# Kernel optimization log

Measured on AMD Instinct MI355X. Metric: run time of the kernel, lower is better.

Reference implementation:

```python
import jax, jax.numpy as jnp
import numpy as np

D = 512      # d_model
P = 128      # proj_len
H = 8        # nhead
MID = 24     # middle_dim (hardcoded in module)
HD = MID // H    # head_dim = 3
HDV = D // H     # head_dim_v = 64
SCALE = HD ** -0.5   # scaling == pscaling since head_dim == phead_dim


def setup_inputs() -> dict:
    key = jax.random.key(0)
    ks = jax.random.split(key, 12)
    L, B = 2048, 16
    def w(k, o, i):
        return jax.random.normal(k, (o, i), jnp.float32) * 0.02
    def b(o):
        return jnp.zeros((o,), jnp.float32)
    return {
        "x": jax.random.normal(ks[0], (L, B, D), jnp.float32),
        "px": jax.random.normal(ks[1], (P, B, D), jnp.float32),
        "mask": jax.random.randint(ks[2], (B, L), 0, 2).astype(bool),
        "Wpq": w(ks[3], MID, D), "bpq": b(MID),
        "Wq": w(ks[4], MID, D), "bq": b(MID),
        "Wql": w(ks[5], P * H, D), "bql": b(P * H),
        "Wpk": w(ks[6], MID, D), "bpk": b(MID),
        "Wpv": w(ks[7], D, D), "bpv": b(D),
        "Wk": w(ks[8], MID, D), "bk": b(MID),
        "Wv": w(ks[9], D, D), "bv": b(D),
        "Wo": w(ks[10], D, D), "bo": b(D),
        "gamma": jnp.ones((D,), jnp.float32),
        "beta": jnp.zeros((D,), jnp.float32),
    }


def _layernorm(x, g, b, eps=1e-5):
    m = x.mean(-1, keepdims=True)
    v = ((x - m) ** 2).mean(-1, keepdims=True)
    return (x - m) / jnp.sqrt(v + eps) * g + b


def reference(x, px, mask, Wpq, bpq, Wq, bq, Wql, bql, Wpk, bpk, Wpv, bpv,
              Wk, bk, Wv, bv, Wo, bo, gamma, beta):
    L, B, _ = x.shape
    BH = B * H
    # ---- stage 1: compress length L -> P via projected attention ----
    pk = (x @ Wpk.T + bpk).reshape(L, BH, HD)     # [L, BH, hd]
    pv = (x @ Wpv.T + bpv).reshape(L, BH, HDV)    # [L, BH, hdv]
    pq = (px @ Wpq.T + bpq).reshape(P, BH, HD) * SCALE
    pqk = jnp.einsum('pnh,lnh->npl', pq, pk)      # [BH, P, L]
    pqk = pqk.reshape(B, H, P, L)
    pqk = jnp.where(mask[:, None, None, :], -jnp.inf, pqk).reshape(BH, P, L)
    pqk = jax.nn.softmax(pqk, axis=-1)            # dropout1 omitted (eval)
    pc = jnp.einsum('npl,lnv->npv', pqk, pv)      # [BH, P, hdv]
    pc = pc.transpose(1, 0, 2).reshape(P, B, D)   # compressed context
    # ---- stage 2: attention within compressed length P ----
    q_len = (x @ Wql.T + bql).reshape(L, BH, P).transpose(1, 0, 2)  # [BH, L, P]
    k = (pc @ Wk.T + bk).reshape(P, BH, HD).transpose(1, 0, 2)      # [BH, P, hd]
    v = (pc @ Wv.T + bv).reshape(P, BH, HDV).transpose(1, 0, 2)     # [BH, P, hdv]
    q = ((pc @ Wq.T + bq) * SCALE).reshape(P, BH, HD).transpose(1, 0, 2)
    aw = jax.nn.softmax(q @ k.transpose(0, 2, 1), axis=-1)  # [BH, P, P], dropout2 omitted
    attn = aw @ v                                            # [BH, P, hdv]
    attn = attn.transpose(1, 0, 2).reshape(P, B, D)
    attn = _layernorm(attn, gamma, beta)
    attn = attn.reshape(P, BH, HDV).transpose(1, 0, 2)       # [BH, P, hdv]
    # ---- stage 3: re-expand P -> L via learned length softmax ----
    ql = jax.nn.softmax(q_len, axis=-1)                      # dropout3 omitted
    out = (ql @ attn).transpose(1, 0, 2).reshape(L, B, D)
    return (out @ Wo.T + bo, pc)
```

## Files before the change

### kernel.cpp

```cpp
#include <hip/hip_runtime.h>
#include <cstdint>

#define L_    2048
#define B_    16
#define D_    512
#define P_    128
#define H_    8
#define MID_  24
#define HD_   3
#define HDV_  64
#define BH_   128
#define SCALE_ 0.57735026918962576f
#define S1C   4
#define S1L   (L_ / S1C)

typedef short  short8  __attribute__((ext_vector_type(8)));
typedef short  short4v __attribute__((ext_vector_type(4)));
typedef float  f32x4   __attribute__((ext_vector_type(4)));

__device__ __forceinline__ short f2bf(float f) {
    unsigned u = __builtin_bit_cast(unsigned, f);
    unsigned r = (u + 0x7fffu + ((u >> 16) & 1u)) >> 16;
    return (short)(unsigned short)r;
}

__device__ __forceinline__ int swz8(int row, int chunk) {
    return row * 64 + ((chunk ^ (row & 7)) << 3);
}

__device__ __forceinline__ int swzP(int row, int g) {
    return row * 128 + ((g ^ (row & 7)) << 3);
}

__device__ __forceinline__ float block_reduce_sum_256(float v, volatile float* scratch) {
#pragma unroll
    for (int o = 32; o > 0; o >>= 1) v += __shfl_down(v, o, 64);
    int wid = threadIdx.x >> 6;
    if ((threadIdx.x & 63) == 0) scratch[wid] = v;
    __syncthreads();
    if (threadIdx.x == 0) scratch[4] = scratch[0] + scratch[1] + scratch[2] + scratch[3];
    __syncthreads();
    return scratch[4];
}

__global__ __launch_bounds__(256) void cvt_bf16(
    const float* __restrict__ src, short* __restrict__ dst, int n4)
{
    int i = blockIdx.x * 256 + threadIdx.x;
    if (i < n4) {
        float4 v = reinterpret_cast<const float4*>(src)[i];
        short4v o;
        o[0] = f2bf(v.x); o[1] = f2bf(v.y); o[2] = f2bf(v.z); o[3] = f2bf(v.w);
        reinterpret_cast<short4v*>(dst)[i] = o;
    }
}

__global__ __launch_bounds__(256) void proj24(
    const float* __restrict__ A, const float* __restrict__ W,
    const float* __restrict__ bias, float* __restrict__ C, float scale)
{
    const int lane = threadIdx.x & 63;
    const int cg   = __builtin_amdgcn_readfirstlane(threadIdx.x >> 6);
    const int row  = blockIdx.x * 64 + lane;
    const int c0   = cg * 6;
    const float* __restrict__ wb = W + (size_t)c0 * D_;
    const float* __restrict__ xr = A + (size_t)row * D_;

    float acc[6] = {0.f, 0.f, 0.f, 0.f, 0.f, 0.f};
    for (int kk = 0; kk < D_; kk += 8) {
        float4 x0 = *reinterpret_cast<const float4*>(xr + kk);
        float4 x1 = *reinterpret_cast<const float4*>(xr + kk + 4);
#pragma unroll
        for (int j = 0; j < 6; ++j) {
            float4 w0 = *reinterpret_cast<const float4*>(wb + j * D_ + kk);
            float4 w1 = *reinterpret_cast<const float4*>(wb + j * D_ + kk + 4);
            acc[j] = fmaf(x0.x, w0.x, fmaf(x0.y, w0.y, fmaf(x0.z, w0.z, fmaf(x0.w, w0.w, acc[j]))));
            acc[j] = fmaf(x1.x, w1.x, fmaf(x1.y, w1.y, fmaf(x1.z, w1.z, fmaf(x1.w, w1.w, acc[j]))));
        }
    }
#pragma unroll
    for (int j = 0; j < 6; ++j)
        C[(size_t)row * MID_ + c0 + j] = (acc[j] + bias[c0 + j]) * scale;
}

__global__ __launch_bounds__(256) void gemm_bias2(
    const float* __restrict__ A,
    const float* __restrict__ W0, const float* __restrict__ b0, float* __restrict__ C0, float s0,
    const float* __restrict__ W1, const float* __restrict__ b1, float* __restrict__ C1, float s1,
    int M, int N, int K)
{
    const float* W    = blockIdx.z ? W1 : W0;
    const float* bias = blockIdx.z ? b1 : b0;
    float*       C    = blockIdx.z ? C1 : C0;
    const float scale = blockIdx.z ? s1 : s0;

    __shared__ float As[32][36];
    __shared__ float Ws[64][36];
    const int t    = threadIdx.x;
    const int row0 = blockIdx.y * 32;
    const int col0 = blockIdx.x * 64;
    const int ty = t >> 4;
    const int tx = t & 15;
    const int lr  = t >> 3;
    const int lc4 = (t & 7) * 4;

    float acc[2][4] = {{0.f,0.f,0.f,0.f},{0.f,0.f,0.f,0.f}};

    for (int kk0 = 0; kk0 < K; kk0 += 32) {
        {
            float4 a = *reinterpret_cast<const float4*>(&A[(size_t)(row0 + lr) * K + kk0 + lc4]);
            *reinterpret_cast<float4*>(&As[lr][lc4]) = a;
        }
#pragma unroll
        for (int i = 0; i < 2; ++i) {
            int wr   = i * 32 + lr;
            int wcol = col0 + wr;
            float4 w = make_float4(0.f, 0.f, 0.f, 0.f);
            if (wcol < N)
                w = *reinterpret_cast<const float4*>(&W[(size_t)wcol * K + kk0 + lc4]);
            *reinterpret_cast<float4*>(&Ws[wr][lc4]) = w;
        }
        __syncthreads();
#pragma unroll
        for (int k4 = 0; k4 < 8; ++k4) {
            float4 a0 = *reinterpret_cast<const float4*>(&As[ty * 2][k4 * 4]);
            float4 a1 = *reinterpret_cast<const float4*>(&As[ty * 2 + 1][k4 * 4]);
#pragma unroll
            for (int ci = 0; ci < 4; ++ci) {
                float4 w = *reinterpret_cast<const float4*>(&Ws[ci * 16 + tx][k4 * 4]);
                acc[0][ci] += a0.x * w.x + a0.y * w.y + a0.z * w.z + a0.w * w.w;
                acc[1][ci] += a1.x * w.x + a1.y * w.y + a1.z * w.z + a1.w * w.w;
            }
        }
        __syncthreads();
    }
#pragma unroll
    for (int ri = 0; ri < 2; ++ri) {
        int r = row0 + ty * 2 + ri;
#pragma unroll
        for (int ci = 0; ci < 4; ++ci) {
            int c = col0 + ci * 16 + tx;
            if (c < N) C[(size_t)r * N + c] = (acc[ri][ci] + bias[c]) * scale;
        }
    }
}

__global__ __launch_bounds__(256) void gemm_mfma_bt(
    const float* __restrict__ A, const short* __restrict__ Wb,
    const float* __restrict__ bias, float* __restrict__ C,
    int M, int N, int K)
{
    __shared__ __align__(16) short As[128][40];
    __shared__ __align__(16) short Bs[64][40];
    const int t    = threadIdx.x;
    const int w    = t >> 6;
    const int lane = t & 63;
    const int q    = lane >> 4;
    const int l16  = lane & 15;
    const int row0 = blockIdx.y * 128;
    const int col0 = blockIdx.x * 64;

    const int ar = t >> 1;
    const int ac = (t & 1) * 16;
    const int br = t >> 2;
    const int bc = (t & 3) * 8;

    const f32x4 z = {0.f, 0.f, 0.f, 0.f};
    f32x4 acc[2][4];
#pragma unroll
    for (int i = 0; i < 2; ++i)
#pragma unroll
        for (int j = 0; j < 4; ++j) acc[i][j] = z;

    for (int kk = 0; kk < K; kk += 32) {
        {
            const float4* ap = reinterpret_cast<const float4*>(&A[(size_t)(row0 + ar) * K + kk + ac]);
            float4 v0 = ap[0], v1 = ap[1], v2 = ap[2], v3 = ap[3];
            short8 s0, s1;
            s0[0]=f2bf(v0.x); s0[1]=f2bf(v0.y); s0[2]=f2bf(v0.z); s0[3]=f2bf(v0.w);
            s0[4]=f2bf(v1.x); s0[5]=f2bf(v1.y); s0[6]=f2bf(v1.z); s0[7]=f2bf(v1.w);
            s1[0]=f2bf(v2.x); s1[1]=f2bf(v2.y); s1[2]=f2bf(v2.z); s1[3]=f2bf(v2.w);
            s1[4]=f2bf(v3.x); s1[5]=f2bf(v3.y); s1[6]=f2bf(v3.z); s1[7]=f2bf(v3.w);
            *reinterpret_cast<short8*>(&As[ar][ac])     = s0;
            *reinterpret_cast<short8*>(&As[ar][ac + 8]) = s1;
        }
        *reinterpret_cast<short8*>(&Bs[br][bc]) =
            *reinterpret_cast<const short8*>(&Wb[(size_t)(col0 + br) * K + kk + bc]);
        __syncthreads();

        short8 af[2], bf[4];
#pragma unroll
        for (int i = 0; i < 2; ++i)
            af[i] = *reinterpret_cast<const short8*>(&As[32 * w + i * 16 + l16][q * 8]);
#pragma unroll
        for (int ct = 0; ct < 4; ++ct)
            bf[ct] = *reinterpret_cast<const short8*>(&Bs[ct * 16 + l16][q * 8]);
#pragma unroll
        for (int i = 0; i < 2; ++i)
#pragma unroll
            for (int ct = 0; ct < 4; ++ct)
                acc[i][ct] = __builtin_amdgcn_mfma_f32_16x16x32_bf16(af[i], bf[ct], acc[i][ct], 0, 0, 0);
        __syncthreads();
    }

#pragma unroll
    for (int i = 0; i < 2; ++i) {
#pragma unroll
        for (int ct = 0; ct < 4; ++ct) {
            int col = col0 + ct * 16 + l16;
            float bv = bias[col];
#pragma unroll
            for (int r = 0; r < 4; ++r) {
                int row = row0 + 32 * w + i * 16 + q * 4 + r;
                C[(size_t)row * N + col] = acc[i][ct][r] + bv;
            }
        }
    }
}

template<bool BF16OUT>
__global__ __launch_bounds__(256) void gemm_bb(
    const short* __restrict__ Ab, const short* __restrict__ Wb,
    const float* __restrict__ bias, void* __restrict__ Cout,
    int M, int N, int K)
{
    __shared__ __align__(16) short As[128 * 64];
    __shared__ __align__(16) short Bs[128 * 64];
    const int t    = threadIdx.x;
    const int w    = t >> 6;
    const int lane = t & 63;
    const int q    = lane >> 4;
    const int l16  = lane & 15;

    const int gid  = blockIdx.x;
    const int nct  = N >> 7;
    const int xcd  = gid & 7;
    const int j    = gid >> 3;
    const int row0 = (xcd + 8 * (j / nct)) * 128;
    const int col0 = (j % nct) * 128;

    const int sr  = t >> 1;
    const int sc0 = (t & 1) * 4;

    const f32x4 z = {0.f, 0.f, 0.f, 0.f};
    f32x4 acc[2][8];
#pragma unroll
    for (int i = 0; i < 2; ++i)
#pragma unroll
        for (int jj = 0; jj < 8; ++jj) acc[i][jj] = z;

    for (int kk = 0; kk < K; kk += 64) {
        {
            const short* ap = &Ab[(size_t)(row0 + sr) * K + kk + sc0 * 8];
            const short* bp = &Wb[(size_t)(col0 + sr) * K + kk + sc0 * 8];
#pragma unroll
            for (int c = 0; c < 4; ++c) {
                *reinterpret_cast<short8*>(&As[swz8(sr, sc0 + c)]) =
                    *reinterpret_cast<const short8*>(ap + c * 8);
                *reinterpret_cast<short8*>(&Bs[swz8(sr, sc0 + c)]) =
                    *reinterpret_cast<const short8*>(bp + c * 8);
            }
        }
        __syncthreads();

        __builtin_amdgcn_s_setprio(1);
#pragma unroll
        for (int s = 0; s < 2; ++s) {
            short8 af[2], bf[8];
#pragma unroll
            for (int i = 0; i < 2; ++i)
                af[i] = *reinterpret_cast<const short8*>(&As[swz8(32 * w + i * 16 + l16, s * 4 + q)]);
#pragma unroll
            for (int ct = 0; ct < 8; ++ct)
                bf[ct] = *reinterpret_cast<const short8*>(&Bs[swz8(ct * 16 + l16, s * 4 + q)]);
#pragma unroll
            for (int i = 0; i < 2; ++i)
#pragma unroll
                for (int ct = 0; ct < 8; ++ct)
                    acc[i][ct] = __builtin_amdgcn_mfma_f32_16x16x32_bf16(af[i], bf[ct], acc[i][ct], 0, 0, 0);
        }
        __builtin_amdgcn_s_setprio(0);
        __syncthreads();
    }

#pragma unroll
    for (int i = 0; i < 2; ++i) {
#pragma unroll
        for (int ct = 0; ct < 8; ++ct) {
            int col = col0 + ct * 16 + l16;
            float bv = bias[col];
#pragma unroll
            for (int r = 0; r < 4; ++r) {
                int row = row0 + 32 * w + i * 16 + q * 4 + r;
                float v = acc[i][ct][r] + bv;
                if (BF16OUT)
                    ((short*)Cout)[(size_t)row * N + col] = f2bf(v);
                else
                    ((float*)Cout)[(size_t)row * N + col] = v;
            }
        }
    }
}

__global__ __launch_bounds__(512) void stage1_split(
    const float* __restrict__ pk, const float* __restrict__ pq,
    const short* __restrict__ pvb, const int* __restrict__ mask,
    float* __restrict__ pc, float* __restrict__ sumtot)
{
    __shared__ float pkt[S1L * 3];
    __shared__ float mka[S1L];
    __shared__ __align__(16) short As[P_][40];
    __shared__ __align__(16) short pvt[32][68];

    const int t = threadIdx.x;
    const int n = blockIdx.x;
    const int c = blockIdx.y;
    const int lbase = c * S1L;
    const int b = n >> 3;
    const int h = n & 7;

    {
        const int l = t;
        const float* pp = &pk[((size_t)(lbase + l) * BH_ + n) * HD_];
        pkt[l * 3 + 0] = pp[0];
        pkt[l * 3 + 1] = pp[1];
        pkt[l * 3 + 2] = pp[2];
        mka[l] = mask[b * L_ + lbase + l] ? -1e30f : 0.f;
    }

    const int p   = t >> 2;
    const int pl8 = (t & 3) * 8;
    const float pq0 = pq[((size_t)p * B_ + b) * MID_ + h * HD_ + 0];
    const float pq1 = pq[((size_t)p * B_ + b) * MID_ + h * HD_ + 1];
    const float pq2 = pq[((size_t)p * B_ + b) * MID_ + h * HD_ + 2];
    __syncthreads();

    const int lane = t & 63;
    const int w    = t >> 6;
    const int q    = lane >> 4;
    const int l16  = lane & 15;
    const int svl  = t >> 4;
    const int svc  = (t & 15) * 4;

    float psum = 0.f;
    const f32x4 z = {0.f, 0.f, 0.f, 0.f};
    f32x4 acc[4] = {z, z, z, z};

    for (int kt = 0; kt < S1L / 32; ++kt) {
        *reinterpret_cast<short4v*>(&pvt[svl][svc]) =
            *reinterpret_cast<const short4v*>(&pvb[((size_t)(lbase + kt * 32 + svl) * BH_ + n) * HDV_ + svc]);
        {
            const float* pb = &pkt[(kt * 32 + pl8) * 3];
            float kv[24], mk[8];
#pragma unroll
            for (int j = 0; j < 6; ++j)
                *reinterpret_cast<float4*>(&kv[j * 4]) = *reinterpret_cast<const float4*>(pb + j * 4);
            *reinterpret_cast<float4*>(&mk[0]) = *reinterpret_cast<const float4*>(&mka[kt * 32 + pl8]);
            *reinterpret_cast<float4*>(&mk[4]) = *reinterpret_cast<const float4*>(&mka[kt * 32 + pl8 + 4]);
            short8 a8;
#pragma unroll
            for (int j = 0; j < 8; ++j) {
                float s = pq0 * kv[j * 3] + pq1 * kv[j * 3 + 1] + pq2 * kv[j * 3 + 2] + mk[j];
                float e = __expf(s);
                psum += e;
                a8[j] = f2bf(e);
            }
            *reinterpret_cast<short8*>(&As[p][pl8]) = a8;
        }
        __syncthreads();

        short8 af = *reinterpret_cast<const short8*>(&As[w * 16 + l16][q * 8]);
#pragma unroll
        for (int ct = 0; ct < 4; ++ct) {
            short8 bf;
#pragma unroll
            for (int j = 0; j < 8; ++j) bf[j] = pvt[q * 8 + j][ct * 16 + l16];
            acc[ct] = __builtin_amdgcn_mfma_f32_16x16x32_bf16(af, bf, acc[ct], 0, 0, 0);
        }
        __syncthreads();
    }

    psum += __shfl_xor(psum, 1, 64);
    psum += __shfl_xor(psum, 2, 64);
    if ((t & 3) == 0) unsafeAtomicAdd(&sumtot[n * P_ + p], psum);

#pragma unroll
    for (int ct = 0; ct < 4; ++ct) {
        int dv = ct * 16 + l16;
#pragma unroll
        for (int r = 0; r < 4; ++r) {
            int pr = w * 16 + q * 4 + r;
            unsafeAtomicAdd(&pc[((size_t)(pr * B_ + b)) * D_ + h * HDV_ + dv], acc[ct][r]);
        }
    }
}

__global__ __launch_bounds__(256) void normalize_pc(
    float* __restrict__ pc, const float* __restrict__ sumtot)
{
    int i = blockIdx.x * 256 + threadIdx.x;
    float4 v = reinterpret_cast<float4*>(pc)[i];
    int flat = i * 4;
    int pb = flat >> 9;
    int d  = flat & 511;
    int p = pb >> 4, b = pb & 15, h = d >> 6;
    float s = 1.f / sumtot[(b * H_ + h) * P_ + p];
    v.x *= s; v.y *= s; v.z *= s; v.w *= s;
    reinterpret_cast<float4*>(pc)[i] = v;
}

__global__ __launch_bounds__(256) void stage2_attn(
    const float* __restrict__ qtmp, const float* __restrict__ ktmp,
    const float* __restrict__ vtmp, float* __restrict__ apre)
{
    __shared__ float S[32][132];
    __shared__ float ks[128][4];
    __shared__ float qs[32][4];
    __shared__ float vs[128][64];
    const int t  = threadIdx.x;
    const int n  = blockIdx.x;
    const int b  = n >> 3;
    const int h  = n & 7;
    const int p0 = blockIdx.y * 32;

    if (t < 128) {
        const float* kr = &ktmp[(size_t)(t * B_ + b) * MID_ + h * HD_];
        ks[t][0] = kr[0]; ks[t][1] = kr[1]; ks[t][2] = kr[2];
    } else if (t < 160) {
        int r = t - 128;
        const float* qr = &qtmp[(size_t)((p0 + r) * B_ + b) * MID_ + h * HD_];
        qs[r][0] = qr[0]; qs[r][1] = qr[1]; qs[r][2] = qr[2];
    }
#pragma unroll
    for (int j = 0; j < 8; ++j) {
        int idx = t + j * 256;
        int r = idx >> 4, c4 = (idx & 15) * 4;
        *reinterpret_cast<float4*>(&vs[r][c4]) =
            *reinterpret_cast<const float4*>(&vtmp[(size_t)(r * B_ + b) * D_ + h * HDV_ + c4]);
    }
    __syncthreads();

    {
        const int c  = t & 127;
        const int rg = t >> 7;
        float k0 = ks[c][0], k1 = ks[c][1], k2 = ks[c][2];
#pragma unroll
        for (int i = 0; i < 16; ++i) {
            int r = rg * 16 + i;
            S[r][c] = qs[r][0] * k0 + qs[r][1] * k1 + qs[r][2] * k2;
        }
    }
    __syncthreads();

    {
        const int srow = t >> 3;
        const int c0   = (t & 7) * 16;
        float mx = -1e30f;
#pragma unroll
        for (int i = 0; i < 16; ++i) mx = fmaxf(mx, S[srow][c0 + i]);
        mx = fmaxf(mx, __shfl_xor(mx, 1, 64));
        mx = fmaxf(mx, __shfl_xor(mx, 2, 64));
        mx = fmaxf(mx, __shfl_xor(mx, 4, 64));
        float e[16];
        float sum = 0.f;
#pragma unroll
        for (int i = 0; i < 16; ++i) { e[i] = __expf(S[srow][c0 + i] - mx); sum += e[i]; }
        sum += __shfl_xor(sum, 1, 64);
        sum += __shfl_xor(sum, 2, 64);
        sum += __shfl_xor(sum, 4, 64);
        float inv = 1.f / sum;
#pragma unroll
        for (int i = 0; i < 16; ++i) S[srow][c0 + i] = e[i] * inv;
    }
    __syncthreads();

    {
        const int dv = t & 63;
        const int pg = t >> 6;
        float acc[8] = {0.f,0.f,0.f,0.f,0.f,0.f,0.f,0.f};
        for (int pp = 0; pp < 128; pp += 4) {
            float v0 = vs[pp + 0][dv], v1 = vs[pp + 1][dv];
            float v2 = vs[pp + 2][dv], v3 = vs[pp + 3][dv];
#pragma unroll
            for (int pi = 0; pi < 8; ++pi) {
                const float4 s4 = *reinterpret_cast<const float4*>(&S[pg * 8 + pi][pp]);
                acc[pi] = fmaf(s4.x, v0, fmaf(s4.y, v1, fmaf(s4.z, v2, fmaf(s4.w, v3, acc[pi]))));
            }
        }
#pragma unroll
        for (int pi = 0; pi < 8; ++pi)
            apre[(size_t)((p0 + pg * 8 + pi) * B_ + b) * D_ + h * HDV_ + dv] = acc[pi];
    }
}

__global__ __launch_bounds__(256) void layernorm_t(
    const float* __restrict__ apre, const float* __restrict__ gamma,
    const float* __restrict__ beta, short* __restrict__ attnT2)
{
    __shared__ float red[8];
    const int t   = threadIdx.x;
    const int row = blockIdx.x;
    const int p   = row >> 4;
    const int b   = row & 15;
    float v0 = apre[(size_t)row * D_ + t];
    float v1 = apre[(size_t)row * D_ + 256 + t];
    float mean = block_reduce_sum_256(v0 + v1, red) * (1.f / D_);
    float d0 = v0 - mean, d1 = v1 - mean;
    float var  = block_reduce_sum_256(d0 * d0 + d1 * d1, red) * (1.f / D_);
    float rstd = rsqrtf(var + 1e-5f);
#pragma unroll
    for (int j = 0; j < 2; ++j) {
        int d = t + j * 256;
        int h = d >> 6, dv = d & 63;
        float v = (j ? d1 : d0) * rstd * gamma[d] + beta[d];
        attnT2[(((size_t)(b * H_ + h)) * HDV_ + dv) * P_ + p] = f2bf(v);
    }
}

__global__ __launch_bounds__(512, 4) void score_pv(
    const short* __restrict__ xb, const short* __restrict__ Wqlb,
    const float* __restrict__ bql, const short* __restrict__ attnT2,
    short* __restrict__ yf)
{
    __shared__ __align__(16) char smraw[128 * 128 * 2];
    short* As = reinterpret_cast<short*>(smraw);
    short* Bs = reinterpret_cast<short*>(smraw + 16384);
    short* Pp = reinterpret_cast<short*>(smraw);
    __shared__ float reds[128][4];
    __shared__ __align__(16) short Vt[64 * 128];

    const int t    = threadIdx.x;
    const int gid  = blockIdx.x;
    const int xcd  = gid & 7;
    const int j    = gid >> 3;
    const int h    = j & 7;
    const int combo = xcd + 8 * (j >> 3);
    const int b    = combo & 15;
    const int l0   = (combo >> 4) * 128;

    const int lane = t & 63;
    const int w    = t >> 6;
    const int q    = lane >> 4;
    const int l16  = lane & 15;
    const int rg   = w & 3;
    const int ch   = w >> 2;
    const int sar  = t >> 2;
    const int sch  = t & 3;

#pragma unroll
    for (int jj = 0; jj < 2; ++jj) {
        int G   = t * 2 + jj;
        int row = G >> 4, g = G & 15;
        *reinterpret_cast<short8*>(&Vt[swzP(row, g)]) =
            *reinterpret_cast<const short8*>(&attnT2[(((size_t)(b * H_ + h)) * HDV_ + row) * P_ + g * 8]);
    }

    const f32x4 z = {0.f, 0.f, 0.f, 0.f};
    f32x4 acc[2][4];
#pragma unroll
    for (int i = 0; i < 2; ++i)
#pragma unroll
        for (int jj = 0; jj < 4; ++jj) acc[i][jj] = z;

    for (int kk = 0; kk < D_; kk += 64) {
        {
            const short* xp = &xb[(size_t)((l0 + sar) * B_ + b) * D_ + kk + sch * 8];
            const short* wp = &Wqlb[(size_t)(h * P_ + sar) * D_ + kk + sch * 8];
            *reinterpret_cast<short8*>(&As[swz8(sar, sch)])     = *reinterpret_cast<const short8*>(xp);
            *reinterpret_cast<short8*>(&As[swz8(sar, sch + 4)]) = *reinterpret_cast<const short8*>(xp + 32);
            *reinterpret_cast<short8*>(&Bs[swz8(sar, sch)])     = *reinterpret_cast<const short8*>(wp);
            *reinterpret_cast<short8*>(&Bs[swz8(sar, sch + 4)]) = *reinterpret_cast<const short8*>(wp + 32);
        }
        __syncthreads();

        __builtin_amdgcn_s_setprio(1);
#pragma unroll
        for (int s = 0; s < 2; ++s) {
            short8 af[2], bf[4];
#pragma unroll
            for (int i = 0; i < 2; ++i)
                af[i] = *reinterpret_cast<const short8*>(&Bs[swz8(rg * 32 + i * 16 + l16, s * 4 + q)]);
#pragma unroll
            for (int ct = 0; ct < 4; ++ct)
                bf[ct] = *reinterpret_cast<const short8*>(&As[swz8(ch * 64 + ct * 16 + l16, s * 4 + q)]);
#pragma unroll
            for (int i = 0; i < 2; ++i)
#pragma unroll
                for (int ct = 0; ct < 4; ++ct)
                    acc[i][ct] = __builtin_amdgcn_mfma_f32_16x16x32_bf16(af[i], bf[ct], acc[i][ct], 0, 0, 0);
        }
        __builtin_amdgcn_s_setprio(0);
        __syncthreads();
    }

    {
        float bv[2][4];
#pragma unroll
        for (int i = 0; i < 2; ++i)
#pragma unroll
            for (int r = 0; r < 4; ++r)
                bv[i][r] = bql[h * P_ + rg * 32 + i * 16 + q * 4 + r];
#pragma unroll
        for (int i = 0; i < 2; ++i)
#pragma unroll
            for (int ct = 0; ct < 4; ++ct)
#pragma unroll
                for (int r = 0; r < 4; ++r)
                    acc[i][ct][r] += bv[i][r];
    }

    float e[4][2][4];
#pragma unroll
    for (int ct = 0; ct < 4; ++ct) {
        float s = 0.f;
#pragma unroll
        for (int i = 0; i < 2; ++i)
#pragma unroll
            for (int r = 0; r < 4; ++r) {
                float v = __expf(acc[i][ct][r]);
                e[ct][i][r] = v;
                s += v;
            }
        s += __shfl_xor(s, 16, 64);
        s += __shfl_xor(s, 32, 64);
        if (q == 0) reds[ch * 64 + ct * 16 + l16][rg] = s;
    }
    __syncthreads();

#pragma unroll
    for (int ct = 0; ct < 4; ++ct) {
        const int lc = ch * 64 + ct * 16 + l16;
        float S   = reds[lc][0] + reds[lc][1] + reds[lc][2] + reds[lc][3];
        float inv = 1.f / S;
#pragma unroll
        for (int i = 0; i < 2; ++i) {
            int p0 = rg * 32 + i * 16 + q * 4;
            short4v o;
#pragma unroll
            for (int r = 0; r < 4; ++r)
                o[r] = f2bf(e[ct][i][r] * inv);
            *reinterpret_cast<short4v*>(&Pp[swzP(lc, p0 >> 3) + (p0 & 7)]) = o;
        }
    }
    __syncthreads();

    {
        f32x4 acc2[4] = {z, z, z, z};
        const int arow = 16 * w + l16;
#pragma unroll
        for (int ks = 0; ks < 4; ++ks) {
            short8 pa = *reinterpret_cast<const short8*>(&Pp[swzP(arow, ks * 4 + q)]);
#pragma unroll
            for (int ct = 0; ct < 4; ++ct) {
                short8 vb = *reinterpret_cast<const short8*>(&Vt[swzP(ct * 16 + l16, ks * 4 + q)]);
                acc2[ct] = __builtin_amdgcn_mfma_f32_16x16x32_bf16(pa, vb, acc2[ct], 0, 0, 0);
            }
        }
#pragma unroll
        for (int ct = 0; ct < 4; ++ct) {
            int dv = ct * 16 + l16;
#pragma unroll
            for (int r = 0; r < 4; ++r) {
                int lrow = 16 * w + q * 4 + r;
                yf[(size_t)((l0 + lrow) * B_ + b) * D_ + h * HDV_ + dv] = f2bf(acc2[ct][r]);
            }
        }
    }
}

extern "C" void kernel_launch(void* const* d_in, const int* in_sizes, int n_in,
                              void* d_out, int out_size, void* d_ws, size_t ws_size,
                              hipStream_t stream)
{
    const float* x     = (const float*)d_in[0];
    const float* px    = (const float*)d_in[1];
    const int*   mask  = (const int*)d_in[2];
    const float* Wpq   = (const float*)d_in[3];
    const float* bpq   = (const float*)d_in[4];
    const float* Wq    = (const float*)d_in[5];
    const float* bq    = (const float*)d_in[6];
    const float* Wql   = (const float*)d_in[7];
    const float* bql   = (const float*)d_in[8];
    const float* Wpk   = (const float*)d_in[9];
    const float* bpk   = (const float*)d_in[10];
    const float* Wpv   = (const float*)d_in[11];
    const float* bpv   = (const float*)d_in[12];
    const float* Wk    = (const float*)d_in[13];
    const float* bk    = (const float*)d_in[14];
    const float* Wv    = (const float*)d_in[15];
    const float* bv    = (const float*)d_in[16];
    const float* Wo    = (const float*)d_in[17];
    const float* bo    = (const float*)d_in[18];
    const float* gamma = (const float*)d_in[19];
    const float* beta  = (const float*)d_in[20];

    float* out = (float*)d_out;
    float* pc  = out + (size_t)L_ * B_ * D_;

    float* ws    = (float*)d_ws;
    float* pk    = ws;
    float* pq    = pk    + 786432;
    float* ktmp  = pq    + 49152;
    float* qtmp  = ktmp  + 49152;
    float* vtmp  = qtmp  + 49152;
    float* apre  = vtmp  + 1048576;
    short* Wpvb  = (short*)(apre + 1048576);
    short* Wob   = Wpvb + 262144;
    short* Wqlb  = Wob  + 262144;
    short* Wvb   = Wqlb + 524288;
    short* xb    = Wvb  + 262144;
    short* pvb   = xb   + 16777216;
    float* sumtot = (float*)(pvb + 16777216);
    short* yf    = pvb;
    short* attnT2 = (short*)pk;

    const int MLB = L_ * B_;
    const int MPB = P_ * B_;

    cvt_bf16<<<dim3(256),   256, 0, stream>>>(Wpv, Wpvb, D_*D_/4);
    cvt_bf16<<<dim3(256),   256, 0, stream>>>(Wo,  Wob,  D_*D_/4);
    cvt_bf16<<<dim3(512),   256, 0, stream>>>(Wql, Wqlb, P_*H_*D_/4);
    cvt_bf16<<<dim3(256),   256, 0, stream>>>(Wv,  Wvb,  D_*D_/4);
    cvt_bf16<<<dim3(16384), 256, 0, stream>>>(x,   xb,   MLB*D_/4);

    hipMemsetAsync(pc, 0, (size_t)P_ * B_ * D_ * sizeof(float), stream);
    hipMemsetAsync(sumtot, 0, (size_t)BH_ * P_ * sizeof(float), stream);

    proj24<<<dim3(MLB / 64), 256, 0, stream>>>(x,  Wpk, bpk, pk, 1.f);
    proj24<<<dim3(MPB / 64), 256, 0, stream>>>(px, Wpq, bpq, pq, SCALE_);
    gemm_bb<true><<<dim3((MLB / 128) * (D_ / 128)), 256, 0, stream>>>(xb, Wpvb, bpv, pvb, MLB, D_, D_);
    stage1_split<<<dim3(BH_, S1C), 512, 0, stream>>>(pk, pq, pvb, mask, pc, sumtot);
    normalize_pc<<<dim3(P_ * B_ * D_ / 4 / 256), 256, 0, stream>>>(pc, sumtot);
    gemm_bias2<<<dim3(1, MPB / 32, 2), 256, 0, stream>>>(pc, Wk, bk, ktmp, 1.f,
                                                          Wq, bq, qtmp, SCALE_, MPB, MID_, D_);
    gemm_mfma_bt<<<dim3(D_ / 64, MPB / 128), 256, 0, stream>>>(pc, Wvb, bv, vtmp, MPB, D_, D_);
    stage2_attn<<<dim3(BH_, 4), 256, 0, stream>>>(qtmp, ktmp, vtmp, apre);
    layernorm_t<<<dim3(MPB), 256, 0, stream>>>(apre, gamma, beta, attnT2);
    score_pv<<<dim3((MLB / 128) * H_), 512, 0, stream>>>(xb, Wqlb, bql, attnT2, yf);
    gemm_bb<false><<<dim3((MLB / 128) * (D_ / 128)), 256, 0, stream>>>(yf, Wob, bo, out, MLB, D_, D_);
}
```

Measured before the change: 434.4 us.

## Fuse x bf16 conversion into proj24 and reorder score_pv staging loads

The standalone conversion kernel for x is removed, and proj24 now writes the bf16 copy of x as it reads each row. One wave converts its row into a swizzled 64KB shared tile, which is then written out coalesced, so x (64 MB in fp32) is read once fewer. Separately, score_pv's shared-memory staging now alternates which 8-element chunk each thread stores first by row parity, intended to cut LDS bank conflicts. The cost is 64KB of shared memory per proj24 block, which lowers occupancy, and a conversion load that falls on only one of the four waves.

```diff
diff --git a/kernel.cpp b/kernel.cpp
--- a/kernel.cpp
+++ b/kernel.cpp
@@ -55,12 +55,16 @@
     }
 }
 
+template<bool CVT>
 __global__ __launch_bounds__(256) void proj24(
     const float* __restrict__ A, const float* __restrict__ W,
-    const float* __restrict__ bias, float* __restrict__ C, float scale)
-{
-    const int lane = threadIdx.x & 63;
-    const int cg   = __builtin_amdgcn_readfirstlane(threadIdx.x >> 6);
+    const float* __restrict__ bias, float* __restrict__ C, float scale,
+    short* __restrict__ Ab)
+{
+    __shared__ short xs[64 * 512];
+    const int t    = threadIdx.x;
+    const int lane = t & 63;
+    const int cg   = __builtin_amdgcn_readfirstlane(t >> 6);
     const int row  = blockIdx.x * 64 + lane;
     const int c0   = cg * 6;
     const float* __restrict__ wb = W + (size_t)c0 * D_;
@@ -70,6 +74,13 @@
     for (int kk = 0; kk < D_; kk += 8) {
         float4 x0 = *reinterpret_cast<const float4*>(xr + kk);
         float4 x1 = *reinterpret_cast<const float4*>(xr + kk + 4);
+        if (CVT && cg == 0) {
+            short8 s;
+            s[0]=f2bf(x0.x); s[1]=f2bf(x0.y); s[2]=f2bf(x0.z); s[3]=f2bf(x0.w);
+            s[4]=f2bf(x1.x); s[5]=f2bf(x1.y); s[6]=f2bf(x1.z); s[7]=f2bf(x1.w);
+            int chunk = kk >> 3;
+            *reinterpret_cast<short8*>(&xs[lane * 512 + ((chunk ^ (lane & 7)) << 3)]) = s;
+        }
 #pragma unroll
         for (int j = 0; j < 6; ++j) {
             float4 w0 = *reinterpret_cast<const float4*>(wb + j * D_ + kk);
@@ -81,6 +92,18 @@
 #pragma unroll
     for (int j = 0; j < 6; ++j)
         C[(size_t)row * MID_ + c0 + j] = (acc[j] + bias[c0 + j]) * scale;
+
+    if (CVT) {
+        __syncthreads();
+#pragma unroll
+        for (int i = 0; i < 16; ++i) {
+            int c  = t + i * 256;
+            int r  = c >> 6;
+            int cl = c & 63;
+            short8 v = *reinterpret_cast<const short8*>(&xs[r * 512 + ((cl ^ (r & 7)) << 3)]);
+            *reinterpret_cast<short8*>(&Ab[(size_t)(blockIdx.x * 64 + r) * D_ + cl * 8]) = v;
+        }
+    }
 }
 
 __global__ __launch_bounds__(256) void gemm_bias2(
@@ -545,7 +568,8 @@
     const int rg   = w & 3;
     const int ch   = w >> 2;
     const int sar  = t >> 2;
-    const int sch  = t & 3;
+    const int c1   = (t & 3) | ((sar & 1) << 2);
+    const int c2   = c1 ^ 4;
 
 #pragma unroll
     for (int jj = 0; jj < 2; ++jj) {
@@ -564,12 +588,12 @@
 
     for (int kk = 0; kk < D_; kk += 64) {
         {
-            const short* xp = &xb[(size_t)((l0 + sar) * B_ + b) * D_ + kk + sch * 8];
-            const short* wp = &Wqlb[(size_t)(h * P_ + sar) * D_ + kk + sch * 8];
-            *reinterpret_cast<short8*>(&As[swz8(sar, sch)])     = *reinterpret_cast<const short8*>(xp);
-            *reinterpret_cast<short8*>(&As[swz8(sar, sch + 4)]) = *reinterpret_cast<const short8*>(xp + 32);
-            *reinterpret_cast<short8*>(&Bs[swz8(sar, sch)])     = *reinterpret_cast<const short8*>(wp);
-            *reinterpret_cast<short8*>(&Bs[swz8(sar, sch + 4)]) = *reinterpret_cast<const short8*>(wp + 32);
+            const short* xp = &xb[(size_t)((l0 + sar) * B_ + b) * D_ + kk];
+            const short* wp = &Wqlb[(size_t)(h * P_ + sar) * D_ + kk];
+            *reinterpret_cast<short8*>(&As[swz8(sar, c1)]) = *reinterpret_cast<const short8*>(xp + c1 * 8);
+            *reinterpret_cast<short8*>(&As[swz8(sar, c2)]) = *reinterpret_cast<const short8*>(xp + c2 * 8);
+            *reinterpret_cast<short8*>(&Bs[swz8(sar, c1)]) = *reinterpret_cast<const short8*>(wp + c1 * 8);
+            *reinterpret_cast<short8*>(&Bs[swz8(sar, c2)]) = *reinterpret_cast<const short8*>(wp + c2 * 8);
         }
         __syncthreads();
 
@@ -721,13 +745,12 @@
     cvt_bf16<<<dim3(256),   256, 0, stream>>>(Wo,  Wob,  D_*D_/4);
     cvt_bf16<<<dim3(512),   256, 0, stream>>>(Wql, Wqlb, P_*H_*D_/4);
     cvt_bf16<<<dim3(256),   256, 0, stream>>>(Wv,  Wvb,  D_*D_/4);
-    cvt_bf16<<<dim3(16384), 256, 0, stream>>>(x,   xb,   MLB*D_/4);
 
     hipMemsetAsync(pc, 0, (size_t)P_ * B_ * D_ * sizeof(float), stream);
     hipMemsetAsync(sumtot, 0, (size_t)BH_ * P_ * sizeof(float), stream);
 
-    proj24<<<dim3(MLB / 64), 256, 0, stream>>>(x,  Wpk, bpk, pk, 1.f);
-    proj24<<<dim3(MPB / 64), 256, 0, stream>>>(px, Wpq, bpq, pq, SCALE_);
+    proj24<true><<<dim3(MLB / 64), 256, 0, stream>>>(x,  Wpk, bpk, pk, 1.f, xb);
+    proj24<false><<<dim3(MPB / 64), 256, 0, stream>>>(px, Wpq, bpq, pq, SCALE_, nullptr);
     gemm_bb<true><<<dim3((MLB / 128) * (D_ / 128)), 256, 0, stream>>>(xb, Wpvb, bpv, pvb, MLB, D_, D_);
     stage1_split<<<dim3(BH_, S1C), 512, 0, stream>>>(pk, pq, pvb, mask, pc, sumtot);
     normalize_pc<<<dim3(P_ * B_ * D_ / 4 / 256), 256, 0, stream>>>(pc, sumtot);
```

Measured after the change: 442.2 us. About the same (+1.8%).
